# Performance work log

Measured on AMD Instinct MI355X. Metric: run time of the kernel, lower is better.

Reference implementation:

```python
import jax, jax.numpy as jnp
import numpy as np

B, T, E = 64, 64, 512
D_MODEL = 2 * E          # 1024, mamba d_model (concat of spatial+temporal)
D_INNER = 2 * D_MODEL    # 2048
D_STATE = 16
DT_RANK = D_MODEL // 16  # 64
K_CONV = 4


def setup_inputs() -> dict:
    key = jax.random.key(0)
    ks = jax.random.split(key, 12)
    def n(k, shape, scale=0.02):
        return jax.random.normal(k, shape, jnp.float32) * scale
    return {
        "spatial_features": jax.random.normal(ks[0], (B, T, E), jnp.float32),
        "temporal_features": jax.random.normal(ks[1], (B, T, E), jnp.float32),
        "W_in": n(ks[2], (D_MODEL, 2 * D_INNER)),
        "conv_w": n(ks[3], (D_INNER, K_CONV)),
        "conv_b": jnp.zeros((D_INNER,), jnp.float32),
        "W_x": n(ks[4], (D_INNER, DT_RANK + 2 * D_STATE)),
        "W_dt": n(ks[5], (DT_RANK, D_INNER)),
        "b_dt": jnp.zeros((D_INNER,), jnp.float32),
        "A_log": n(ks[6], (D_INNER, D_STATE)),   # A = -exp(A_log) ~ -1
        "D_skip": jnp.ones((D_INNER,), jnp.float32),
        "W_out": n(ks[7], (D_INNER, D_MODEL)),
        "W1": n(ks[8], (D_MODEL, 512)),
        "b1": jnp.zeros((512,), jnp.float32),
        "W2": n(ks[9], (512, 256)),
        "b2": jnp.zeros((256,), jnp.float32),
        "W3": n(ks[10], (256, 6)),
        "b3": jnp.zeros((6,), jnp.float32),
    }


def _mamba(x, W_in, conv_w, conv_b, W_x, W_dt, b_dt, A_log, D_skip, W_out):
    # x: (B, T, d_model) -> (B, T, d_model). Standard Mamba selective-scan block.
    Bsz = x.shape[0]
    xz = jnp.einsum('btd,de->bte', x, W_in)            # (B,T,2*d_inner)
    xi, z = jnp.split(xz, 2, axis=-1)
    # causal depthwise conv1d over T
    xt = jnp.pad(jnp.swapaxes(xi, 1, 2), ((0, 0), (0, 0), (K_CONV - 1, 0)))
    conv = jax.lax.conv_general_dilated(
        xt, conv_w[:, None, :], (1,), 'VALID', feature_group_count=D_INNER)
    xc = jax.nn.silu(jnp.swapaxes(conv, 1, 2) + conv_b)  # (B,T,d_inner)
    proj = jnp.einsum('btd,de->bte', xc, W_x)            # (B,T,dt_rank+2n)
    dt_raw, Bs, Cs = jnp.split(proj, [DT_RANK, DT_RANK + D_STATE], axis=-1)
    dt = jax.nn.softplus(jnp.einsum('btr,rd->btd', dt_raw, W_dt) + b_dt)
    A = -jnp.exp(A_log)                                  # (d_inner, n)

    def step(h, inputs):
        dt_t, B_t, C_t, x_t = inputs                     # (B,d),(B,n),(B,n),(B,d)
        dA = jnp.exp(dt_t[..., None] * A)                # (B,d,n)
        h = dA * h + (dt_t * x_t)[..., None] * B_t[:, None, :]
        y = jnp.einsum('bdn,bn->bd', h, C_t)
        return h, y

    xs = (jnp.swapaxes(dt, 0, 1), jnp.swapaxes(Bs, 0, 1),
          jnp.swapaxes(Cs, 0, 1), jnp.swapaxes(xc, 0, 1))
    h0 = jnp.zeros((Bsz, D_INNER, D_STATE), xc.dtype)
    _, ys = jax.lax.scan(step, h0, xs)
    y = jnp.swapaxes(ys, 0, 1) + xc * D_skip
    y = y * jax.nn.silu(z)
    return jnp.einsum('btd,de->bte', y, W_out)


def reference(spatial_features, temporal_features, W_in, conv_w, conv_b, W_x,
              W_dt, b_dt, A_log, D_skip, W_out, W1, b1, W2, b2, W3, b3):
    # concat -> final Mamba -> per-frame MLP head (vectorized over B,T)
    x = jnp.concatenate([spatial_features, temporal_features], axis=-1)  # (B,T,2E)
    f = _mamba(x, W_in, conv_w, conv_b, W_x, W_dt, b_dt, A_log, D_skip, W_out)
    h1 = jax.nn.relu(f @ W1 + b1)
    h2 = jax.nn.relu(h1 @ W2 + b2)
    return h2 @ W3 + b3  # (B,T,6)
```

## Files before the change

kernel.cpp:

```cpp
#include <hip/hip_runtime.h>
#include <hip/hip_bf16.h>
#include <math.h>

#define B_   64
#define T_   64
#define E_   512
#define DM   1024
#define DI   2048
#define DS   16
#define DTR  64
#define M_   4096

typedef __hip_bfloat16 bf16;
typedef __attribute__((ext_vector_type(8))) short bf16x8;
typedef __attribute__((ext_vector_type(4))) float f32x4;

template<int ACT, int OUTBF, int SPLITK, int BM, int BN, int ATOMIC = 0>
__global__ __launch_bounds__(256) void gemm_mfma(
    const bf16* __restrict__ A, int lda,
    const bf16* __restrict__ Bt, int ldb,
    void* __restrict__ Cv, int ldc,
    const float* __restrict__ bias,
    int Ndim, int Kdim)
{
    __shared__ __align__(16) bf16 As[BM * 32];
    __shared__ __align__(16) bf16 Bs[BN * 32];
    const int tid  = threadIdx.x;
    const int wave = tid >> 6;
    const int lane = tid & 63;
    const int bm = blockIdx.y * BM;
    const int bn = blockIdx.x * BN;
    const int lrow = lane >> 2;
    const int lkc  = (lane & 3) * 8;
    constexpr int RPW = (BM + BN) / 4;
    constexpr int NI  = RPW / 16;
    constexpr int WMT = BM / 32;
    constexpr int WNT = BN / 32;
    const int wm = (wave >> 1) * (BM / 2);
    const int wn = (wave & 1) * (BN / 2);
    const int fm = lane & 15;
    const int fq = lane >> 4;

    int kstart = 0, kend = Kdim;
    if (SPLITK > 1) {
        int chunk = Kdim / SPLITK;
        kstart = blockIdx.z * chunk;
        kend = kstart + chunk;
    }

    f32x4 acc[WMT][WNT];
    #pragma unroll
    for (int i = 0; i < WMT; ++i)
        #pragma unroll
        for (int j = 0; j < WNT; ++j)
            acc[i][j] = (f32x4){0.f, 0.f, 0.f, 0.f};

    for (int k0 = kstart; k0 < kend; k0 += 32) {
        #pragma unroll
        for (int i = 0; i < NI; ++i) {
            int rowbase = wave * RPW + i * 16;
            int row = rowbase + lrow;
            if (rowbase < BM) {
                const bf16* ga = A + (size_t)(bm + row) * lda + k0 + lkc;
                __builtin_amdgcn_global_load_lds(
                    (const __attribute__((address_space(1))) void*)ga,
                    (__attribute__((address_space(3))) void*)&As[rowbase * 32],
                    16, 0, 0);
            } else {
                int brow = bn + row - BM;
                if (brow >= Ndim) brow = Ndim - 1;
                const bf16* gb = Bt + (size_t)brow * ldb + k0 + lkc;
                __builtin_amdgcn_global_load_lds(
                    (const __attribute__((address_space(1))) void*)gb,
                    (__attribute__((address_space(3))) void*)&Bs[(rowbase - BM) * 32],
                    16, 0, 0);
            }
        }
        __syncthreads();
        bf16x8 a[WMT], b[WNT];
        #pragma unroll
        for (int i = 0; i < WMT; ++i)
            a[i] = *(const bf16x8*)&As[(wm + i * 16 + fm) * 32 + fq * 8];
        #pragma unroll
        for (int j = 0; j < WNT; ++j)
            b[j] = *(const bf16x8*)&Bs[(wn + j * 16 + fm) * 32 + fq * 8];
        #pragma unroll
        for (int i = 0; i < WMT; ++i)
            #pragma unroll
            for (int j = 0; j < WNT; ++j)
                acc[i][j] = __builtin_amdgcn_mfma_f32_16x16x32_bf16(
                    a[i], b[j], acc[i][j], 0, 0, 0);
        __syncthreads();
    }

    size_t zoff = (SPLITK > 1 && !ATOMIC) ? (size_t)blockIdx.z * M_ * ldc : 0;
    #pragma unroll
    for (int i = 0; i < WMT; ++i) {
        int rowb = bm + wm + i * 16 + fq * 4;
        #pragma unroll
        for (int j = 0; j < WNT; ++j) {
            int col = bn + wn + j * 16 + fm;
            if (col < Ndim) {
                float bv = bias ? bias[col] : 0.f;
                #pragma unroll
                for (int r = 0; r < 4; ++r) {
                    float v = acc[i][j][r] + bv;
                    if (ACT == 1) v = fmaxf(v, 0.f);
                    if (ACT == 2) v = (v > 20.f) ? v : __logf(1.f + __expf(v));
                    size_t off = (size_t)(rowb + r) * ldc + col;
                    if (ATOMIC)          atomicAdd(&((float*)Cv)[off], v);
                    else if (SPLITK > 1) ((float*)Cv)[zoff + off] = v;
                    else if (OUTBF)      ((bf16*)Cv)[off] = __float2bfloat16(v);
                    else                 ((float*)Cv)[off] = v;
                }
            }
        }
    }
}

__global__ __launch_bounds__(256) void gemm_g1_conv(
    const bf16* __restrict__ A,
    const bf16* __restrict__ Bt,
    bf16* __restrict__ xcb,
    bf16* __restrict__ zb,
    const float* __restrict__ conv_w,
    const float* __restrict__ conv_b)
{
    constexpr int XS = 136;
    __shared__ __align__(16) bf16 smem[128 * XS];
    const int tid  = threadIdx.x;
    const int wave = tid >> 6;
    const int lane = tid & 63;
    const int bm = blockIdx.y * 128;
    const int bn = blockIdx.x * 128;
    const int lrow = lane >> 2;
    const int lkc  = (lane & 3) * 8;
    const int wm = (wave >> 1) * 64;
    const int wn = (wave & 1) * 64;
    const int fm = lane & 15;
    const int fq = lane >> 4;

    f32x4 acc[4][4];
    #pragma unroll
    for (int i = 0; i < 4; ++i)
        #pragma unroll
        for (int j = 0; j < 4; ++j)
            acc[i][j] = (f32x4){0.f, 0.f, 0.f, 0.f};

    for (int k0 = 0; k0 < 1024; k0 += 32) {
        #pragma unroll
        for (int i = 0; i < 4; ++i) {
            int rowbase = wave * 64 + i * 16;
            int row = rowbase + lrow;
            if (rowbase < 128) {
                const bf16* ga = A + (size_t)(bm + row) * 1024 + k0 + lkc;
                __builtin_amdgcn_global_load_lds(
                    (const __attribute__((address_space(1))) void*)ga,
                    (__attribute__((address_space(3))) void*)&smem[rowbase * 32],
                    16, 0, 0);
            } else {
                const bf16* gb = Bt + (size_t)(bn + row - 128) * 1024 + k0 + lkc;
                __builtin_amdgcn_global_load_lds(
                    (const __attribute__((address_space(1))) void*)gb,
                    (__attribute__((address_space(3))) void*)&smem[4096 + (rowbase - 128) * 32],
                    16, 0, 0);
            }
        }
        __syncthreads();
        bf16x8 a[4], b[4];
        #pragma unroll
        for (int i = 0; i < 4; ++i)
            a[i] = *(const bf16x8*)&smem[(wm + i * 16 + fm) * 32 + fq * 8];
        #pragma unroll
        for (int j = 0; j < 4; ++j)
            b[j] = *(const bf16x8*)&smem[4096 + (wn + j * 16 + fm) * 32 + fq * 8];
        #pragma unroll
        for (int i = 0; i < 4; ++i)
            #pragma unroll
            for (int j = 0; j < 4; ++j)
                acc[i][j] = __builtin_amdgcn_mfma_f32_16x16x32_bf16(
                    a[i], b[j], acc[i][j], 0, 0, 0);
        __syncthreads();
    }

    if (bn < 2048) {
        #pragma unroll
        for (int i = 0; i < 4; ++i) {
            int rowb = wm + i * 16 + fq * 4;
            #pragma unroll
            for (int j = 0; j < 4; ++j) {
                int col = wn + j * 16 + fm;
                #pragma unroll
                for (int r = 0; r < 4; ++r)
                    smem[(rowb + r) * XS + col] = __float2bfloat16(acc[i][j][r]);
            }
        }
        __syncthreads();
        {
            int col = tid & 127;
            int seq = tid >> 7;
            int gcol = bn + col;
            float4 cw = *(const float4*)&conv_w[gcol * 4];
            float cb = conv_b[gcol];
            float w0 = 0.f, w1 = 0.f, w2 = 0.f;
            int base = seq * 64;
            for (int t = 0; t < 64; ++t) {
                int idx = (base + t) * XS + col;
                float cur = __bfloat162float(smem[idx]);
                float cacc = cb;
                cacc = fmaf(w0, cw.x, cacc); cacc = fmaf(w1, cw.y, cacc);
                cacc = fmaf(w2, cw.z, cacc); cacc = fmaf(cur, cw.w, cacc);
                smem[idx] = __float2bfloat16(__fdividef(cacc, 1.f + __expf(-cacc)));
                w0 = w1; w1 = w2; w2 = cur;
            }
        }
        __syncthreads();
        #pragma unroll
        for (int it = 0; it < 8; ++it) {
            int g = it * 256 + tid;
            int row = g >> 4;
            int cg = (g & 15) * 8;
            bf16x8 v = *(const bf16x8*)&smem[row * XS + cg];
            *(bf16x8*)&xcb[(size_t)(bm + row) * 2048 + bn + cg] = v;
        }
    } else {
        #pragma unroll
        for (int i = 0; i < 4; ++i) {
            int rowb = bm + wm + i * 16 + fq * 4;
            #pragma unroll
            for (int j = 0; j < 4; ++j) {
                int col = bn - 2048 + wn + j * 16 + fm;
                #pragma unroll
                for (int r = 0; r < 4; ++r)
                    zb[(size_t)(rowb + r) * 2048 + col] =
                        __float2bfloat16(acc[i][j][r]);
            }
        }
    }
}

__global__ __launch_bounds__(256) void gemm_g3(
    const float* __restrict__ proj,
    const bf16* __restrict__ WdT,
    bf16* __restrict__ dtb,
    const float* __restrict__ b_dt)
{
    __shared__ __align__(16) bf16 As[128 * 32];
    __shared__ __align__(16) bf16 Bs[64 * 32];
    const int tid  = threadIdx.x;
    const int wave = tid >> 6;
    const int lane = tid & 63;
    const int bm = blockIdx.y * 128;
    const int bn = blockIdx.x * 64;
    const int lrow = lane >> 2;
    const int lkc  = (lane & 3) * 8;
    const int wm = (wave >> 1) * 64;
    const int wn = (wave & 1) * 32;
    const int fm = lane & 15;
    const int fq = lane >> 4;
    const int arow = tid >> 1;
    const int akh  = (tid & 1) * 16;

    f32x4 acc[4][2];
    #pragma unroll
    for (int i = 0; i < 4; ++i)
        #pragma unroll
        for (int j = 0; j < 2; ++j)
            acc[i][j] = (f32x4){0.f, 0.f, 0.f, 0.f};

    #pragma unroll
    for (int k0 = 0; k0 < 64; k0 += 32) {
        {
            const bf16* gb = WdT + (size_t)(bn + wave * 16 + lrow) * 64 + k0 + lkc;
            __builtin_amdgcn_global_load_lds(
                (const __attribute__((address_space(1))) void*)gb,
                (__attribute__((address_space(3))) void*)&Bs[wave * 16 * 32],
                16, 0, 0);
        }
        {
            const float* ga = proj + (size_t)(bm + arow) * 96 + k0 + akh;
            float4 v0 = *(const float4*)(ga + 0);
            float4 v1 = *(const float4*)(ga + 4);
            float4 v2 = *(const float4*)(ga + 8);
            float4 v3 = *(const float4*)(ga + 12);
            bf16 o[16] = {
                __float2bfloat16(v0.x), __float2bfloat16(v0.y),
                __float2bfloat16(v0.z), __float2bfloat16(v0.w),
                __float2bfloat16(v1.x), __float2bfloat16(v1.y),
                __float2bfloat16(v1.z), __float2bfloat16(v1.w),
                __float2bfloat16(v2.x), __float2bfloat16(v2.y),
                __float2bfloat16(v2.z), __float2bfloat16(v2.w),
                __float2bfloat16(v3.x), __float2bfloat16(v3.y),
                __float2bfloat16(v3.z), __float2bfloat16(v3.w)};
            *(bf16x8*)&As[arow * 32 + akh]     = *(const bf16x8*)&o[0];
            *(bf16x8*)&As[arow * 32 + akh + 8] = *(const bf16x8*)&o[8];
        }
        __syncthreads();
        bf16x8 a[4], b[2];
        #pragma unroll
        for (int i = 0; i < 4; ++i)
            a[i] = *(const bf16x8*)&As[(wm + i * 16 + fm) * 32 + fq * 8];
        #pragma unroll
        for (int j = 0; j < 2; ++j)
            b[j] = *(const bf16x8*)&Bs[(wn + j * 16 + fm) * 32 + fq * 8];
        #pragma unroll
        for (int i = 0; i < 4; ++i)
            #pragma unroll
            for (int j = 0; j < 2; ++j)
                acc[i][j] = __builtin_amdgcn_mfma_f32_16x16x32_bf16(
                    a[i], b[j], acc[i][j], 0, 0, 0);
        __syncthreads();
    }

    #pragma unroll
    for (int i = 0; i < 4; ++i) {
        int rowb = bm + wm + i * 16 + fq * 4;
        #pragma unroll
        for (int j = 0; j < 2; ++j) {
            int col = bn + wn + j * 16 + fm;
            float bv = b_dt[col];
            #pragma unroll
            for (int r = 0; r < 4; ++r) {
                float v = acc[i][j][r] + bv;
                v = (v > 20.f) ? v : __logf(1.f + __expf(v));
                dtb[(size_t)(rowb + r) * 2048 + col] = __float2bfloat16(v);
            }
        }
    }
}

template<int P, int RELU, int NCOL>
__global__ __launch_bounds__(256) void redp_kernel(
    const float* __restrict__ parts, int stride,
    const float* __restrict__ bias, bf16* __restrict__ out)
{
    int i4 = blockIdx.x * 256 + threadIdx.x;
    int i = i4 * 4;
    float4 s = *(const float4*)(parts + i);
    #pragma unroll
    for (int p = 1; p < P; ++p) {
        float4 v = *(const float4*)(parts + (size_t)p * stride + i);
        s.x += v.x; s.y += v.y; s.z += v.z; s.w += v.w;
    }
    if (NCOL > 0) {
        int c = i & (NCOL - 1);
        s.x += bias[c]; s.y += bias[c + 1]; s.z += bias[c + 2]; s.w += bias[c + 3];
    }
    if (RELU) {
        s.x = fmaxf(s.x, 0.f); s.y = fmaxf(s.y, 0.f);
        s.z = fmaxf(s.z, 0.f); s.w = fmaxf(s.w, 0.f);
    }
    bf16 o[4] = {__float2bfloat16(s.x), __float2bfloat16(s.y),
                 __float2bfloat16(s.z), __float2bfloat16(s.w)};
    *(short4*)&out[i] = *(short4*)o;
}

__global__ __launch_bounds__(256) void prep_kernel(
    const float* __restrict__ sp, const float* __restrict__ tp,
    bf16* __restrict__ xb, float* __restrict__ proj,
    const float* __restrict__ W_in,  bf16* __restrict__ WinT,
    const float* __restrict__ W_out, bf16* __restrict__ Wob,
    const float* __restrict__ W_x,   bf16* __restrict__ WxT,
    const float* __restrict__ W_dt,  bf16* __restrict__ WdT,
    const float* __restrict__ W1,    bf16* __restrict__ W1T,
    const float* __restrict__ W2,    bf16* __restrict__ W2T)
{
    __shared__ float tile[32][33];
    const int b = blockIdx.x;
    const int tid = threadIdx.x;
    if (b < 4096) {
        int idx = b * 256 + tid;
        int row = idx >> 8;
        int c4 = (idx & 255) * 4;
        const float* src = (c4 < 512) ? (sp + (size_t)row * 512 + c4)
                                      : (tp + (size_t)row * 512 + (c4 - 512));
        float4 v = *(const float4*)src;
        bf16* dst = xb + (size_t)row * 1024 + c4;
        dst[0] = __float2bfloat16(v.x); dst[1] = __float2bfloat16(v.y);
        dst[2] = __float2bfloat16(v.z); dst[3] = __float2bfloat16(v.w);
        if (idx < 98304)
            *(float4*)(proj + (size_t)idx * 4) = make_float4(0.f, 0.f, 0.f, 0.f);
        return;
    }
    if (b < 6144) {
        int idx = (b - 4096) * 1024 + tid * 4;
        float4 v = *(const float4*)(W_out + idx);
        bf16 o[4] = {__float2bfloat16(v.x), __float2bfloat16(v.y),
                     __float2bfloat16(v.z), __float2bfloat16(v.w)};
        *(short4*)&Wob[idx] = *(short4*)o;
        return;
    }
    const float* W; bf16* Wt; int K, N, tb;
    if      (b < 6336) { W = W_x;  Wt = WxT;  K = 2048; N = 96;   tb = b - 6144; }
    else if (b < 6464) { W = W_dt; Wt = WdT;  K = 64;   N = 2048; tb = b - 6336; }
    else if (b < 6976) { W = W1;   Wt = W1T;  K = 1024; N = 512;  tb = b - 6464; }
    else if (b < 7104) { W = W2;   Wt = W2T;  K = 512;  N = 256;  tb = b - 6976; }
    else               { W = W_in; Wt = WinT; K = 1024; N = 4096; tb = b - 7104; }
    int nb = N / 32;
    int bn = (tb % nb) * 32, bk = (tb / nb) * 32;
    int tx = tid & 31, ty = tid >> 5;
    #pragma unroll
    for (int i = 0; i < 32; i += 8)
        tile[ty + i][tx] = W[(size_t)(bk + ty + i) * N + bn + tx];
    __syncthreads();
    #pragma unroll
    for (int i = 0; i < 32; i += 8)
        Wt[(size_t)(bn + ty + i) * K + bk + tx] = __float2bfloat16(tile[tx][ty + i]);
}

__global__ __launch_bounds__(256) void scan_kernel(
    const float* __restrict__ proj,
    const bf16*  __restrict__ dtb,
    bf16* __restrict__ xcy,
    const bf16*  __restrict__ zb,
    const float* __restrict__ A_log,
    const float* __restrict__ D_skip)
{
    __shared__ float BC[64][32];
    const int tid = threadIdx.x;
    const int b = blockIdx.y;
    for (int i = tid; i < 64 * 32; i += 256) {
        int t = i >> 5, c = i & 31;
        BC[t][c] = proj[(size_t)(b * 64 + t) * 96 + 64 + c];
    }
    __syncthreads();

    const int d = blockIdx.x * 256 + tid;
    float av[16];
    const float4* alp = (const float4*)(A_log + d * 16);
    *(float4*)&av[0]  = alp[0];
    *(float4*)&av[4]  = alp[1];
    *(float4*)&av[8]  = alp[2];
    *(float4*)&av[12] = alp[3];
    float A[16];
    #pragma unroll
    for (int n = 0; n < 16; ++n) A[n] = -__expf(av[n]);
    const float Dv = D_skip[d];
    float h[16];
    #pragma unroll
    for (int n = 0; n < 16; ++n) h[n] = 0.f;

    #pragma unroll 2
    for (int t = 0; t < T_; ++t) {
        int row = b * T_ + t;
        size_t off = (size_t)row * DI + d;
        float xv = __bfloat162float(xcy[off]);
        float dt = __bfloat162float(dtb[off]);
        float dtx = dt * xv;
        float y = 0.f;
        #pragma unroll
        for (int n = 0; n < 16; ++n) {
            float dA = __expf(dt * A[n]);
            h[n] = fmaf(dA, h[n], dtx * BC[t][n]);
            y = fmaf(h[n], BC[t][16 + n], y);
        }
        float sk = fmaf(xv, Dv, y);
        float z = __bfloat162float(zb[off]);
        float g = __fdividef(z, 1.f + __expf(-z));
        xcy[off] = __float2bfloat16(sk * g);
    }
}

template<int P>
__global__ __launch_bounds__(256) void head_kernel(
    const float* __restrict__ p6, int stride,
    const float* __restrict__ b2,
    const float* __restrict__ W3, const float* __restrict__ b3,
    float* __restrict__ out)
{
    int row = blockIdx.x * 4 + (threadIdx.x >> 6);
    int lane = threadIdx.x & 63;
    float acc[6] = {0.f, 0.f, 0.f, 0.f, 0.f, 0.f};
    #pragma unroll
    for (int kk = 0; kk < 4; ++kk) {
        int c = lane + kk * 64;
        size_t off = (size_t)row * 256 + c;
        float s = p6[off];
        #pragma unroll
        for (int p = 1; p < P; ++p) s += p6[(size_t)p * stride + off];
        s = fmaxf(s + b2[c], 0.f);
        #pragma unroll
        for (int n = 0; n < 6; ++n) acc[n] = fmaf(s, W3[c * 6 + n], acc[n]);
    }
    #pragma unroll
    for (int n = 0; n < 6; ++n) {
        float v = acc[n];
        #pragma unroll
        for (int off = 32; off > 0; off >>= 1) v += __shfl_down(v, off);
        if (lane == 0) out[(size_t)row * 6 + n] = v + b3[n];
    }
}

extern "C" void kernel_launch(void* const* d_in, const int* in_sizes, int n_in,
                              void* d_out, int out_size, void* d_ws, size_t ws_size,
                              hipStream_t stream)
{
    const float* spatial  = (const float*)d_in[0];
    const float* temporal = (const float*)d_in[1];
    const float* W_in     = (const float*)d_in[2];
    const float* conv_w   = (const float*)d_in[3];
    const float* conv_b   = (const float*)d_in[4];
    const float* W_x      = (const float*)d_in[5];
    const float* W_dt     = (const float*)d_in[6];
    const float* b_dt     = (const float*)d_in[7];
    const float* A_log    = (const float*)d_in[8];
    const float* D_skip   = (const float*)d_in[9];
    const float* W_out    = (const float*)d_in[10];
    const float* W1       = (const float*)d_in[11];
    const float* b1       = (const float*)d_in[12];
    const float* W2       = (const float*)d_in[13];
    const float* b2       = (const float*)d_in[14];
    const float* W3       = (const float*)d_in[15];
    const float* b3       = (const float*)d_in[16];
    float* out = (float*)d_out;

    char* w = (char*)d_ws;
    bf16*  xcb  = (bf16*)(w);
    bf16*  zb   = (bf16*)(w + 16777216);
    bf16*  dtb  = (bf16*)(w + 33554432);
    float* p5   = (float*)(w + 33554432);
    float* p6   = (float*)(w + 33554432);
    bf16*  xb   = (bf16*)(w + 67108864);
    bf16*  WinT = (bf16*)(w + 75497472);
    bf16*  WcT  = (bf16*)(w + 83886080);
    bf16*  W1T  = (bf16*)(w + 88080384);
    bf16*  W2T  = (bf16*)(w + 89128960);
    bf16*  WxT  = (bf16*)(w + 89391104);
    bf16*  WdT  = (bf16*)(w + 89784320);
    float* proj = (float*)(w + 90046464);
    bf16*  h1   = (bf16*)(w + 91619328);
    bf16*  Wob  = (bf16*)(w + 95813632);

    dim3 blk(256);

    prep_kernel<<<dim3(11200), blk, 0, stream>>>(
        spatial, temporal, xb, proj, W_in, WinT, W_out, Wob,
        W_x, WxT, W_dt, WdT, W1, W1T, W2, W2T);

    gemm_mfma<0, 1, 1, 128, 64><<<dim3(32, 4), blk, 0, stream>>>(
        W1T, 1024, Wob, 1024, WcT, 2048, nullptr, 2048, 1024);

    gemm_g1_conv<<<dim3(32, 32), blk, 0, stream>>>(
        xb, WinT, xcb, zb, conv_w, conv_b);

    gemm_mfma<0, 0, 8, 128, 128, 1><<<dim3(1, 32, 8), blk, 0, stream>>>(
        xcb, 2048, WxT, 2048, proj, 96, nullptr, 96, 2048);

    gemm_g3<<<dim3(32, 32), blk, 0, stream>>>(proj, WdT, dtb, b_dt);

    scan_kernel<<<dim3(8, 64), blk, 0, stream>>>(
        proj, dtb, xcb, zb, A_log, D_skip);

    gemm_mfma<0, 0, 4, 128, 128><<<dim3(4, 32, 4), blk, 0, stream>>>(
        xcb, 2048, WcT, 2048, p5, 512, nullptr, 512, 2048);

    redp_kernel<4, 1, 512><<<dim3(2048), blk, 0, stream>>>(
        p5, 2097152, b1, h1);

    gemm_mfma<0, 0, 4, 128, 128><<<dim3(2, 32, 4), blk, 0, stream>>>(
        h1, 512, W2T, 512, p6, 256, nullptr, 256, 512);

    head_kernel<4><<<dim3(1024), blk, 0, stream>>>(
        p6, 1048576, b2, W3, b3, out);
}
```

Before: 305.0 us.

## Fold W1·W_out weight-combine GEMM into in_proj conv kernel grid; halve split-K

The separate launch that precomputes the combined W_out·W1 weight matrix is merged into the in_proj+conv GEMM kernel. Four extra column blocks in the grid run that small GEMM, which removes one launch and lets it overlap with the main GEMM. The later GEMM that produces the first head layer drops from split-K 4 to split-K 2, which halves the partial-sum traffic in the reduction kernel but gives fewer blocks for parallelism.

```diff
diff --git a/kernel.cpp b/kernel.cpp
--- a/kernel.cpp
+++ b/kernel.cpp
@@ -124,21 +124,86 @@
     bf16* __restrict__ xcb,
     bf16* __restrict__ zb,
     const float* __restrict__ conv_w,
-    const float* __restrict__ conv_b)
+    const float* __restrict__ conv_b,
+    const bf16* __restrict__ W1T,
+    const bf16* __restrict__ Wob,
+    bf16* __restrict__ WcT)
 {
     constexpr int XS = 136;
     __shared__ __align__(16) bf16 smem[128 * XS];
     const int tid  = threadIdx.x;
     const int wave = tid >> 6;
     const int lane = tid & 63;
-    const int bm = blockIdx.y * 128;
-    const int bn = blockIdx.x * 128;
     const int lrow = lane >> 2;
     const int lkc  = (lane & 3) * 8;
     const int wm = (wave >> 1) * 64;
-    const int wn = (wave & 1) * 64;
     const int fm = lane & 15;
     const int fq = lane >> 4;
+
+    if (blockIdx.x >= 32) {
+        const int fbm = (blockIdx.x - 32) * 128;
+        const int fbn = blockIdx.y * 64;
+        const int fwn = (wave & 1) * 32;
+        f32x4 facc[4][2];
+        #pragma unroll
+        for (int i = 0; i < 4; ++i)
+            #pragma unroll
+            for (int j = 0; j < 2; ++j)
+                facc[i][j] = (f32x4){0.f, 0.f, 0.f, 0.f};
+
+        for (int k0 = 0; k0 < 1024; k0 += 32) {
+            #pragma unroll
+            for (int i = 0; i < 3; ++i) {
+                int rowbase = wave * 48 + i * 16;
+                int row = rowbase + lrow;
+                if (rowbase < 128) {
+                    const bf16* ga = W1T + (size_t)(fbm + row) * 1024 + k0 + lkc;
+                    __builtin_amdgcn_global_load_lds(
+                        (const __attribute__((address_space(1))) void*)ga,
+                        (__attribute__((address_space(3))) void*)&smem[rowbase * 32],
+                        16, 0, 0);
+                } else {
+                    const bf16* gb = Wob + (size_t)(fbn + row - 128) * 1024 + k0 + lkc;
+                    __builtin_amdgcn_global_load_lds(
+                        (const __attribute__((address_space(1))) void*)gb,
+                        (__attribute__((address_space(3))) void*)&smem[4096 + (rowbase - 128) * 32],
+                        16, 0, 0);
+                }
+            }
+            __syncthreads();
+            bf16x8 a[4], b[2];
+            #pragma unroll
+            for (int i = 0; i < 4; ++i)
+                a[i] = *(const bf16x8*)&smem[(wm + i * 16 + fm) * 32 + fq * 8];
+            #pragma unroll
+            for (int j = 0; j < 2; ++j)
+                b[j] = *(const bf16x8*)&smem[4096 + (fwn + j * 16 + fm) * 32 + fq * 8];
+            #pragma unroll
+            for (int i = 0; i < 4; ++i)
+                #pragma unroll
+                for (int j = 0; j < 2; ++j)
+                    facc[i][j] = __builtin_amdgcn_mfma_f32_16x16x32_bf16(
+                        a[i], b[j], facc[i][j], 0, 0, 0);
+            __syncthreads();
+        }
+        #pragma unroll
+        for (int i = 0; i < 4; ++i) {
+            int rowb = fbm + wm + i * 16 + fq * 4;
+            #pragma unroll
+            for (int j = 0; j < 2; ++j) {
+                int col = fbn + fwn + j * 16 + fm;
+                #pragma unroll
+                for (int r = 0; r < 4; ++r)
+                    WcT[(size_t)(rowb + r) * 2048 + col] =
+                        __float2bfloat16(facc[i][j][r]);
+            }
+        }
+        return;
+    }
+
+    const int bm = blockIdx.y * 128;
+    const int bn = blockIdx.x * 128;
+    const int wn = (wave & 1) * 64;
 
     f32x4 acc[4][4];
     #pragma unroll
@@ -537,11 +602,8 @@
         spatial, temporal, xb, proj, W_in, WinT, W_out, Wob,
         W_x, WxT, W_dt, WdT, W1, W1T, W2, W2T);
 
-    gemm_mfma<0, 1, 1, 128, 64><<<dim3(32, 4), blk, 0, stream>>>(
-        W1T, 1024, Wob, 1024, WcT, 2048, nullptr, 2048, 1024);
-
-    gemm_g1_conv<<<dim3(32, 32), blk, 0, stream>>>(
-        xb, WinT, xcb, zb, conv_w, conv_b);
+    gemm_g1_conv<<<dim3(36, 32), blk, 0, stream>>>(
+        xb, WinT, xcb, zb, conv_w, conv_b, W1T, Wob, WcT);
 
     gemm_mfma<0, 0, 8, 128, 128, 1><<<dim3(1, 32, 8), blk, 0, stream>>>(
         xcb, 2048, WxT, 2048, proj, 96, nullptr, 96, 2048);
@@ -551,10 +613,10 @@
     scan_kernel<<<dim3(8, 64), blk, 0, stream>>>(
         proj, dtb, xcb, zb, A_log, D_skip);
 
-    gemm_mfma<0, 0, 4, 128, 128><<<dim3(4, 32, 4), blk, 0, stream>>>(
+    gemm_mfma<0, 0, 2, 128, 128><<<dim3(4, 32, 2), blk, 0, stream>>>(
         xcb, 2048, WcT, 2048, p5, 512, nullptr, 512, 2048);
 
-    redp_kernel<4, 1, 512><<<dim3(2048), blk, 0, stream>>>(
+    redp_kernel<2, 1, 512><<<dim3(2048), blk, 0, stream>>>(
         p5, 2097152, b1, h1);
 
     gemm_mfma<0, 0, 4, 128, 128><<<dim3(2, 32, 4), blk, 0, stream>>>(
```

After: 299.0 us. -2.0%, faster.
